# Optimization experiments

Measured on AMD Instinct MI355X. Metric: run time of the kernel, lower is better.

## Reference

```python
import jax, jax.numpy as jnp
import numpy as np

COST_CLASS, COST_BBOX, COST_GIOU = 2.0, 5.0, 2.0
ALPHA, GAMMA, EPS = 0.25, 2.0, 1e-8


def box_cxcywh_to_xyxy(x):
    cx, cy, w, h = x[..., 0], x[..., 1], x[..., 2], x[..., 3]
    return jnp.stack([cx - 0.5 * w, cy - 0.5 * h, cx + 0.5 * w, cy + 0.5 * h], axis=-1)


def generalized_box_iou(b1, b2):
    # b1: [N,4], b2: [M,4] in xyxy -> [N,M]
    a1 = (b1[:, 2] - b1[:, 0]) * (b1[:, 3] - b1[:, 1])
    a2 = (b2[:, 2] - b2[:, 0]) * (b2[:, 3] - b2[:, 1])
    lt = jnp.maximum(b1[:, None, :2], b2[None, :, :2])
    rb = jnp.minimum(b1[:, None, 2:], b2[None, :, 2:])
    wh = jnp.maximum(rb - lt, 0.0)
    inter = wh[..., 0] * wh[..., 1]
    union = a1[:, None] + a2[None, :] - inter
    iou = inter / jnp.maximum(union, 1e-6)
    elt = jnp.minimum(b1[:, None, :2], b2[None, :, :2])
    erb = jnp.maximum(b1[:, None, 2:], b2[None, :, 2:])
    ewh = jnp.maximum(erb - elt, 0.0)
    encl = ewh[..., 0] * ewh[..., 1]
    return iou - (encl - union) / jnp.maximum(encl, 1e-6)


def setup_inputs() -> dict:
    key = jax.random.key(0)
    k1, k2, k3, k4 = jax.random.split(key, 4)
    bs, nq, nc, nt = 16, 900, 80, 3200
    return {
        'pred_logits': jax.random.normal(k1, (bs, nq, nc), dtype=jnp.float32),
        'pred_boxes': jax.random.uniform(k2, (bs, nq, 4), dtype=jnp.float32),
        'tgt_labels': jax.random.randint(k3, (nt,), 0, nc, dtype=jnp.int32),
        'tgt_boxes': jax.random.uniform(k4, (nt, 4), dtype=jnp.float32),
    }


def reference(pred_logits, pred_boxes, tgt_labels, tgt_boxes):
    bs, nq, nc = pred_logits.shape
    out_prob = jax.nn.sigmoid(pred_logits.reshape(bs * nq, nc))  # [N, C]
    out_bbox = pred_boxes.reshape(bs * nq, 4)                    # [N, 4]

    p = out_prob[:, tgt_labels]  # [N, M] gather by target class
    neg_cost = (1.0 - ALPHA) * p ** GAMMA * (-jnp.log(1.0 - p + EPS))
    pos_cost = ALPHA * (1.0 - p) ** GAMMA * (-jnp.log(p + EPS))
    cost_class = pos_cost - neg_cost

    # L1 cdist: [N, M]
    cost_bbox = jnp.sum(jnp.abs(out_bbox[:, None, :] - tgt_boxes[None, :, :]), axis=-1)

    cost_giou = -generalized_box_iou(box_cxcywh_to_xyxy(out_bbox), box_cxcywh_to_xyxy(tgt_boxes))

    C = COST_BBOX * cost_bbox + COST_CLASS * cost_class + COST_GIOU * cost_giou
    C = jnp.nan_to_num(C, nan=1.0)
    return C.reshape(bs, nq, -1)
```

## Files before the change

### kernel.cpp

```cpp
#include <hip/hip_runtime.h>
#include <cmath>

#define NCC   80
#define QT    8
#define BLK   256
#define VT    4
#define NT_C  3200
#define NQB_C 14400
#define CPR   (NT_C / VT)
#define NRG   (NQB_C / QT)
#define CSTR  20

typedef float f32x4 __attribute__((ext_vector_type(4)));

__device__ __forceinline__ float cls_cost(float x) {
    const float p   = 1.0f / (1.0f + __expf(-x));
    const float om  = 1.0f - p;
    const float pos = 0.25f * om * om * (-__logf(p  + 1e-8f));
    const float neg = 0.75f * p  * p  * (-__logf(om + 1e-8f));
    return 2.0f * (pos - neg) + 2.0f;
}

__global__ __launch_bounds__(BLK) void cost_fast(
    const float* __restrict__ logits,
    const float* __restrict__ pboxes,
    const int*   __restrict__ labels,
    const float* __restrict__ tboxes,
    float*       __restrict__ out)
{
    __shared__ float4 s_clsv[NCC * (CSTR / 4)];
    __shared__ float4 s_qb[2 * QT];
    __shared__ float4 s_qx[2 * QT];
    __shared__ float  s_qa[2 * QT];
    float* s_cls = (float*)s_clsv;

    const int  w0  = blockIdx.x * BLK;
    const int  rg0 = w0 / CPR;
    const bool two = (((w0 + BLK - 1) / CPR) != rg0);

    if (two) {
        for (int t = threadIdx.x; t < 2 * QT * NCC; t += BLK) {
            const int lab = t >> 4, qi = t & 15;
            const int row = (rg0 + (qi >> 3)) * QT + (qi & 7);
            s_cls[lab * CSTR + qi] = cls_cost(logits[row * NCC + lab]);
        }
    } else {
        for (int t = threadIdx.x; t < QT * NCC; t += BLK) {
            const int lab = t >> 3, qi = t & 7;
            const int row = rg0 * QT + qi;
            s_cls[lab * CSTR + qi] = cls_cost(logits[row * NCC + lab]);
        }
    }
    const int ng = two ? 2 * QT : QT;
    if (threadIdx.x < ng) {
        const int rg = rg0 + (threadIdx.x >> 3);
        const float4 b = ((const float4*)pboxes)[rg * QT + (threadIdx.x & 7)];
        s_qb[threadIdx.x] = b;
        s_qx[threadIdx.x] = make_float4(b.x - 0.5f * b.z, b.y - 0.5f * b.w,
                                        b.x + 0.5f * b.z, b.y + 0.5f * b.w);
        s_qa[threadIdx.x] = b.z * b.w;
    }
    __syncthreads();

    const int w  = w0 + threadIdx.x;
    const int rg = w / CPR;
    const int c  = w - rg * CPR;
    const int j  = c * VT;
    const int g8 = (rg - rg0) * QT;

    const int4 lab4 = ((const int4*)labels)[c];
    const int labk[VT] = { lab4.x, lab4.y, lab4.z, lab4.w };
    float4 tb[VT];
    float tx0[VT], ty0[VT], tx1[VT], ty1[VT], ta[VT];
#pragma unroll
    for (int k = 0; k < VT; ++k) {
        tb[k]  = ((const float4*)tboxes)[j + k];
        tx0[k] = tb[k].x - 0.5f * tb[k].z;  tx1[k] = tb[k].x + 0.5f * tb[k].z;
        ty0[k] = tb[k].y - 0.5f * tb[k].w;  ty1[k] = tb[k].y + 0.5f * tb[k].w;
        ta[k]  = tb[k].z * tb[k].w;
    }

    const unsigned obase = (unsigned)(rg * QT) * NT_C + (unsigned)j;

#pragma unroll 1
    for (int h = 0; h < 2; ++h) {
        const int qbase = g8 + h * 4;
        float4 c2v[VT];
#pragma unroll
        for (int k = 0; k < VT; ++k)
            c2v[k] = *(const float4*)&s_cls[labk[k] * CSTR + qbase];

        const unsigned offh = obase + (unsigned)h * 4u * NT_C;
#pragma unroll
        for (int q4 = 0; q4 < 4; ++q4) {
            const int    qi = qbase + q4;
            const float4 qb = s_qb[qi];
            const float4 qx = s_qx[qi];
            const float  qa = s_qa[qi];
            float res[VT];
#pragma unroll
            for (int k = 0; k < VT; ++k) {
                const float c2 = c2v[k][q4];
                const float dx = fminf(qx.z, tx1[k]) - fmaxf(qx.x, tx0[k]);
                const float dy = fminf(qx.w, ty1[k]) - fmaxf(qx.y, ty0[k]);
                const float iw = fmaxf(dx, 0.0f);
                const float ih = fmaxf(dy, 0.0f);
                const float inter = iw * ih;
                const float uni   = (qa + ta[k]) - inter;
                const float ew = (qb.z + tb[k].z) - dx;
                const float eh = (qb.w + tb[k].w) - dy;
                const float encl = ew * eh;
                const float r1 = __builtin_amdgcn_rcpf(fmaxf(uni,  1e-6f));
                const float r2 = __builtin_amdgcn_rcpf(fmaxf(encl, 1e-6f));
                const float l1 = (fabsf(qb.x - tb[k].x) + fabsf(qb.y - tb[k].y))
                               + (fabsf(qb.z - tb[k].z) + fabsf(qb.w - tb[k].w));
                float cc = fmaf(5.0f, l1, c2);
                cc = fmaf(-2.0f * inter, r1, cc);
                cc = fmaf(-2.0f * uni,  r2, cc);
                res[k] = cc;
            }
            f32x4 v = { res[0], res[1], res[2], res[3] };
            __builtin_nontemporal_store(
                v, (f32x4*)(out + offh + (unsigned)q4 * NT_C));
        }
    }
}

__global__ __launch_bounds__(BLK) void cost_generic(
    const float* __restrict__ logits, const float* __restrict__ pboxes,
    const int* __restrict__ labels, const float* __restrict__ tboxes,
    float* __restrict__ out, int NQB, int NT, int NC)
{
    extern __shared__ float smem[];
    float*  s_cls = smem;
    float4* s_qb  = (float4*)(smem + QT * NC);

    const int i0 = blockIdx.y * QT;
    const int j  = blockIdx.x * BLK + threadIdx.x;

    for (int t = threadIdx.x; t < QT * NC; t += BLK) {
        const int qi = i0 + t / NC;
        float v = 0.0f;
        if (qi < NQB) {
            const float x  = logits[qi * NC + (t % NC)];
            const float p  = 1.0f / (1.0f + __expf(-x));
            const float om = 1.0f - p;
            v = 0.25f * om * om * (-__logf(p + 1e-8f))
              - 0.75f * p * p * (-__logf(om + 1e-8f));
        }
        s_cls[t] = v;
    }
    if (threadIdx.x < QT) {
        const int qi = i0 + threadIdx.x;
        s_qb[threadIdx.x] = (qi < NQB) ? ((const float4*)pboxes)[qi]
                                       : make_float4(0.f, 0.f, 0.f, 0.f);
    }
    __syncthreads();
    if (j >= NT) return;

    const float4 tb = ((const float4*)tboxes)[j];
    const int   lab = labels[j];
    const float tx0 = tb.x - 0.5f * tb.z, tx1 = tb.x + 0.5f * tb.z;
    const float ty0 = tb.y - 0.5f * tb.w, ty1 = tb.y + 0.5f * tb.w;
    const float ta  = tb.z * tb.w;

#pragma unroll
    for (int q = 0; q < QT; ++q) {
        const float4 qb = s_qb[q];
        const float ccls = s_cls[q * NC + lab];
        const float l1 = fabsf(qb.x - tb.x) + fabsf(qb.y - tb.y)
                       + fabsf(qb.z - tb.z) + fabsf(qb.w - tb.w);
        const float qx0 = qb.x - 0.5f * qb.z, qx1 = qb.x + 0.5f * qb.z;
        const float qy0 = qb.y - 0.5f * qb.w, qy1 = qb.y + 0.5f * qb.w;
        const float qa  = qb.z * qb.w;
        const float ltx = fmaxf(qx0, tx0), lty = fmaxf(qy0, ty0);
        const float rbx = fminf(qx1, tx1), rby = fminf(qy1, ty1);
        const float iw = fmaxf(rbx - ltx, 0.f), ih = fmaxf(rby - lty, 0.f);
        const float inter = iw * ih;
        const float uni   = qa + ta - inter;
        const float iou   = inter * __builtin_amdgcn_rcpf(fmaxf(uni, 1e-6f));
        const float ex0 = fminf(qx0, tx0), ey0 = fminf(qy0, ty0);
        const float ex1 = fmaxf(qx1, tx1), ey1 = fmaxf(qy1, ty1);
        const float ew = fmaxf(ex1 - ex0, 0.f), eh = fmaxf(ey1 - ey0, 0.f);
        const float encl = ew * eh;
        const float giou = iou - (encl - uni) * __builtin_amdgcn_rcpf(fmaxf(encl, 1e-6f));
        float cc = 5.0f * l1 + 2.0f * ccls - 2.0f * giou;
        cc = (cc == cc) ? cc : 1.0f;
        const int qi = i0 + q;
        if (qi < NQB) out[(size_t)qi * NT + j] = cc;
    }
}

extern "C" void kernel_launch(void* const* d_in, const int* in_sizes, int n_in,
                              void* d_out, int out_size, void* d_ws, size_t ws_size,
                              hipStream_t stream) {
    const float* logits = (const float*)d_in[0];
    const float* pboxes = (const float*)d_in[1];
    const int*   labels = (const int*)d_in[2];
    const float* tboxes = (const float*)d_in[3];
    float*       out    = (float*)d_out;

    const int nqb = in_sizes[1] / 4;
    const int nt  = in_sizes[2];
    const int nc  = in_sizes[0] / nqb;

    if (nqb == NQB_C && nt == NT_C && nc == NCC) {
        const int nblk = (NRG * CPR) / BLK;
        hipLaunchKernelGGL(cost_fast, dim3(nblk), dim3(BLK), 0, stream,
                           logits, pboxes, labels, tboxes, out);
    } else {
        dim3 grid((nt + BLK - 1) / BLK, (nqb + QT - 1) / QT);
        size_t sm = QT * nc * sizeof(float) + QT * sizeof(float4);
        hipLaunchKernelGGL(cost_generic, grid, dim3(BLK), sm, stream,
                           logits, pboxes, labels, tboxes, out, nqb, nt, nc);
    }
}
```

Measured before the change: 56.11 us.

## Precompute class cost table in separate kernel and merge GIoU reciprocals

Adds a prepass kernel that computes the sigmoid/focal class cost once per logit into workspace. The main kernel then loads 16 precomputed rows per block instead of recomputing exp/log each time blocks overlap a query group, and it always loads 16 rows, which removes the branch. It also merges the two reciprocals in the GIoU term into one reciprocal of the product. This adds a second launch and a 4.6MB workspace round trip, and the product of the clamped denominators could lose precision or underflow.

Result: slower. 58.87 us (+4.9%).

```diff
diff --git a/kernel.cpp b/kernel.cpp
--- a/kernel.cpp
+++ b/kernel.cpp
@@ -21,7 +21,15 @@
     return 2.0f * (pos - neg) + 2.0f;
 }
 
+__global__ __launch_bounds__(256) void cls_table_kernel(
+    const float* __restrict__ logits, float* __restrict__ tbl)
+{
+    const int i = blockIdx.x * 256 + threadIdx.x;
+    tbl[i] = cls_cost(logits[i]);
+}
+
 __global__ __launch_bounds__(BLK) void cost_fast(
+    const float* __restrict__ tbl,
     const float* __restrict__ logits,
     const float* __restrict__ pboxes,
     const int*   __restrict__ labels,
@@ -34,27 +42,28 @@
     __shared__ float  s_qa[2 * QT];
     float* s_cls = (float*)s_clsv;
 
-    const int  w0  = blockIdx.x * BLK;
-    const int  rg0 = w0 / CPR;
-    const bool two = (((w0 + BLK - 1) / CPR) != rg0);
-
-    if (two) {
-        for (int t = threadIdx.x; t < 2 * QT * NCC; t += BLK) {
-            const int lab = t >> 4, qi = t & 15;
-            const int row = (rg0 + (qi >> 3)) * QT + (qi & 7);
+    const int w0   = blockIdx.x * BLK;
+    const int rg0  = w0 / CPR;
+    const int row0 = rg0 * QT;
+
+    if (tbl != nullptr) {
+        for (int t = threadIdx.x; t < 16 * NCC; t += BLK) {
+            const int qi  = t / NCC;
+            const int lab = t - qi * NCC;
+            const int row = min(row0 + qi, NQB_C - 1);
+            s_cls[lab * CSTR + qi] = tbl[row * NCC + lab];
+        }
+    } else {
+        for (int t = threadIdx.x; t < 16 * NCC; t += BLK) {
+            const int qi  = t / NCC;
+            const int lab = t - qi * NCC;
+            const int row = min(row0 + qi, NQB_C - 1);
             s_cls[lab * CSTR + qi] = cls_cost(logits[row * NCC + lab]);
         }
-    } else {
-        for (int t = threadIdx.x; t < QT * NCC; t += BLK) {
-            const int lab = t >> 3, qi = t & 7;
-            const int row = rg0 * QT + qi;
-            s_cls[lab * CSTR + qi] = cls_cost(logits[row * NCC + lab]);
-        }
-    }
-    const int ng = two ? 2 * QT : QT;
-    if (threadIdx.x < ng) {
-        const int rg = rg0 + (threadIdx.x >> 3);
-        const float4 b = ((const float4*)pboxes)[rg * QT + (threadIdx.x & 7)];
+    }
+    if (threadIdx.x < 2 * QT) {
+        const int row = min(row0 + (int)threadIdx.x, NQB_C - 1);
+        const float4 b = ((const float4*)pboxes)[row];
         s_qb[threadIdx.x] = b;
         s_qx[threadIdx.x] = make_float4(b.x - 0.5f * b.z, b.y - 0.5f * b.w,
                                         b.x + 0.5f * b.z, b.y + 0.5f * b.w);
@@ -110,13 +119,14 @@
                 const float ew = (qb.z + tb[k].z) - dx;
                 const float eh = (qb.w + tb[k].w) - dy;
                 const float encl = ew * eh;
-                const float r1 = __builtin_amdgcn_rcpf(fmaxf(uni,  1e-6f));
-                const float r2 = __builtin_amdgcn_rcpf(fmaxf(encl, 1e-6f));
+                const float ug  = fmaxf(uni,  1e-6f);
+                const float eg  = fmaxf(encl, 1e-6f);
+                const float num = fmaf(uni, ug, inter * eg);
+                const float r   = __builtin_amdgcn_rcpf(ug * eg);
                 const float l1 = (fabsf(qb.x - tb[k].x) + fabsf(qb.y - tb[k].y))
                                + (fabsf(qb.z - tb[k].z) + fabsf(qb.w - tb[k].w));
                 float cc = fmaf(5.0f, l1, c2);
-                cc = fmaf(-2.0f * inter, r1, cc);
-                cc = fmaf(-2.0f * uni,  r2, cc);
+                cc = fmaf(num * r, -2.0f, cc);
                 res[k] = cc;
             }
             f32x4 v = { res[0], res[1], res[2], res[3] };
@@ -205,9 +215,16 @@
     const int nc  = in_sizes[0] / nqb;
 
     if (nqb == NQB_C && nt == NT_C && nc == NCC) {
+        const size_t tbl_bytes = (size_t)NQB_C * NCC * sizeof(float);
+        float* tbl = nullptr;
+        if (ws_size >= tbl_bytes) {
+            tbl = (float*)d_ws;
+            hipLaunchKernelGGL(cls_table_kernel, dim3((NQB_C * NCC) / 256),
+                               dim3(256), 0, stream, logits, tbl);
+        }
         const int nblk = (NRG * CPR) / BLK;
         hipLaunchKernelGGL(cost_fast, dim3(nblk), dim3(BLK), 0, stream,
-                           logits, pboxes, labels, tboxes, out);
+                           tbl, logits, pboxes, labels, tboxes, out);
     } else {
         dim3 grid((nt + BLK - 1) / BLK, (nqb + QT - 1) / QT);
         size_t sm = QT * nc * sizeof(float) + QT * sizeof(float4);
```
